# Kernel optimization log

Hardware: AMD Instinct MI355X
Metric: run time of the kernel (lower is better)

## Reference

```python
import jax, jax.numpy as jnp
import numpy as np

BN_EPS = 1e-5
DIM = 256
RED = 4
KH, KW = 3, 3


def setup_inputs() -> dict:
    key = jax.random.key(0)
    ks = jax.random.split(key, 4)
    b, c, h, w = 32, DIM, 64, 64
    hid = DIM // RED
    x = jax.random.normal(ks[0], (b, c, h, w), dtype=jnp.float32)
    # 1x1 convs are just matmuls on pooled [b, c] vectors; store as [out, in]
    w1 = jax.random.normal(ks[1], (hid, c), dtype=jnp.float32) * (1.0 / np.sqrt(c))
    bn_gamma = jnp.ones((hid,), dtype=jnp.float32)
    bn_beta = jnp.zeros((hid,), dtype=jnp.float32)
    bn_mean = jnp.zeros((hid,), dtype=jnp.float32)
    bn_var = jnp.ones((hid,), dtype=jnp.float32)
    w2 = jax.random.normal(ks[2], (c * KH * KW, hid), dtype=jnp.float32) * (1.0 / np.sqrt(hid))
    b2 = jnp.zeros((c * KH * KW,), dtype=jnp.float32)
    bias = jnp.zeros((c,), dtype=jnp.float32)
    return {"x": x, "w1": w1, "bn_gamma": bn_gamma, "bn_beta": bn_beta,
            "bn_mean": bn_mean, "bn_var": bn_var, "w2": w2, "b2": b2, "bias": bias}


def reference(x, w1, bn_gamma, bn_beta, bn_mean, bn_var, w2, b2, bias):
    b, c, h, w = x.shape
    # --- SE-style dynamic weight generation ---
    pooled = jnp.mean(x, axis=(2, 3))                      # [b, c]
    y = jnp.einsum('bc,rc->br', pooled, w1)                # conv1 (1x1, no bias)
    y = (y - bn_mean) * jax.lax.rsqrt(bn_var + BN_EPS) * bn_gamma + bn_beta
    y = jax.nn.sigmoid(y)                                  # note: relu is defined but unused in forward
    dyn = jnp.einsum('br,kr->bk', y, w2) + b2              # [b, c*KH*KW]
    dyn = dyn.reshape(b * c, 1, KH, KW)                    # per-sample depthwise kernels (OIHW)
    # --- per-sample depthwise conv via batch-as-groups trick ---
    out = jax.lax.conv_general_dilated(
        x.reshape(1, b * c, h, w), dyn,
        window_strides=(1, 1), padding=((1, 1), (1, 1)),
        feature_group_count=b * c,
        dimension_numbers=('NCHW', 'OIHW', 'NCHW'))
    out = out.reshape(b, c, h, w) + bias[None, :, None, None]
    return out
```

## Files before the change

### kernel.cpp

```cpp
#include <hip/hip_runtime.h>
#include <hip/hip_bf16.h>

#define DIM 256
#define HID 64
#define HW 4096
#define KK 2304
#define LW 72

typedef float f4 __attribute__((ext_vector_type(4)));

__device__ __forceinline__ int skew_of(int R) {
    int r3 = R & 3;
    int g = (r3 & 2) ? r3 : 0;
    return ((R >> 2) + g) & 3;
}

__global__ __launch_bounds__(256) void pool_kernel(const float* __restrict__ x,
                                                   float* __restrict__ pooled) {
    int plane = blockIdx.x;
    const float4* p = (const float4*)(x + (size_t)plane * HW);
    int tid = threadIdx.x;
    float s = 0.f;
#pragma unroll
    for (int k = 0; k < 4; ++k) {
        float4 v = p[tid + k * 256];
        s += (v.x + v.y) + (v.z + v.w);
    }
#pragma unroll
    for (int off = 32; off > 0; off >>= 1) s += __shfl_down(s, off, 64);
    __shared__ float ws[4];
    int wid = tid >> 6, lane = tid & 63;
    if (lane == 0) ws[wid] = s;
    __syncthreads();
    if (tid == 0) {
        float t = (ws[0] + ws[1]) + (ws[2] + ws[3]);
        pooled[plane] = t * (1.0f / (float)HW);
    }
}

__global__ __launch_bounds__(64) void sig_kernel(const float* __restrict__ pooled,
                                                 const float* __restrict__ w1,
                                                 const float* __restrict__ gamma,
                                                 const float* __restrict__ beta,
                                                 const float* __restrict__ mean,
                                                 const float* __restrict__ var,
                                                 float* __restrict__ sigg) {
    int b = blockIdx.x;
    int t = threadIdx.x;
    __shared__ float sp[DIM];
    ((float4*)sp)[t] = ((const float4*)(pooled + b * DIM))[t];
    __syncthreads();
    const float4* wr = (const float4*)(w1 + t * DIM);
    const float4* s4 = (const float4*)sp;
    float acc = 0.f;
#pragma unroll
    for (int i = 0; i < DIM / 4; ++i) {
        float4 v = wr[i]; float4 u = s4[i];
        acc += v.x * u.x + v.y * u.y + v.z * u.z + v.w * u.w;
    }
    float yb = (acc - mean[t]) * rsqrtf(var[t] + 1e-5f) * gamma[t] + beta[t];
    sigg[b * HID + t] = 1.0f / (1.0f + expf(-yb));
}

__global__ __launch_bounds__(256) void conv_kernel(const float* __restrict__ x,
                                                   const float* __restrict__ sigg,
                                                   const float* __restrict__ w2,
                                                   const float* __restrict__ b2,
                                                   const float* __restrict__ bias,
                                                   float* __restrict__ out) {
    int plane = blockIdx.x;
    int c = plane & (DIM - 1);
    int b = plane >> 8;
    int tid = threadIdx.x;
    const float* xp = x + (size_t)plane * HW;

    __shared__ float lds[66 * LW];
    __shared__ float wsh[12];

    const f4* xp4 = (const f4*)xp;
    f4 st[4];
#pragma unroll
    for (int k = 0; k < 4; ++k) st[k] = __builtin_nontemporal_load(&xp4[tid + k * 256]);

    if (tid < 9) {
        int kk = c * 9 + tid;
        const float4* wk = (const float4*)(w2 + (size_t)kk * HID);
        const float4* sg = (const float4*)(sigg + b * HID);
        float acc = b2[kk];
#pragma unroll
        for (int i = 0; i < HID / 4; ++i) {
            float4 v = wk[i]; float4 u = sg[i];
            acc += v.x * u.x + v.y * u.y + v.z * u.z + v.w * u.w;
        }
        wsh[tid] = acc;
    }

    for (int i = tid; i < 272; i += 256) {
        int addr;
        if (i < 72)        addr = i;
        else if (i < 144)  addr = 65 * LW + (i - 72);
        else {
            int z = i - 144;
            int R = 1 + (z >> 1);
            addr = R * LW + skew_of(R) + 3 + (z & 1) * 65;
        }
        lds[addr] = 0.f;
    }

#pragma unroll
    for (int k = 0; k < 4; ++k) {
        int idx = tid + k * 256;
        int R = (idx >> 4) + 1;
        int col0 = (idx & 15) * 4;
        float* dst = &lds[R * LW + skew_of(R) + 4 + col0];
        dst[0] = st[k].x; dst[1] = st[k].y; dst[2] = st[k].z; dst[3] = st[k].w;
    }
    __syncthreads();

    float w[9];
#pragma unroll
    for (int i = 0; i < 9; ++i) w[i] = wsh[i];
    float bv = bias[c];

    int u = tid >> 4, j = tid & 15;
    float acc[4][4];
#pragma unroll
    for (int m = 0; m < 4; ++m)
#pragma unroll
        for (int i = 0; i < 4; ++i) acc[m][i] = bv;

#define CONTRIB(m, t)                                                          \
    {                                                                          \
        float w0 = w[(t)*3 + 0], w1v = w[(t)*3 + 1], w2v = w[(t)*3 + 2];       \
        acc[m][0] += w0 * a0 + w1v * a1 + w2v * a2;                            \
        acc[m][1] += w0 * a1 + w1v * a2 + w2v * a3;                            \
        acc[m][2] += w0 * a2 + w1v * a3 + w2v * a4;                            \
        acc[m][3] += w0 * a3 + w1v * a4 + w2v * a5;                            \
    }
#define READROW(d)                                                             \
    float a0, a1, a2, a3, a4, a5;                                              \
    {                                                                          \
        int R = 4 * u + (d);                                                   \
        const float* r = &lds[R * LW + skew_of(R) + 3 + 4 * j];                \
        a0 = r[0]; a1 = r[1]; a2 = r[2]; a3 = r[3]; a4 = r[4]; a5 = r[5];      \
    }

    { READROW(0) CONTRIB(0, 0) }
    { READROW(1) CONTRIB(0, 1) CONTRIB(1, 0) }
    { READROW(2) CONTRIB(0, 2) CONTRIB(1, 1) CONTRIB(2, 0) }
    { READROW(3) CONTRIB(1, 2) CONTRIB(2, 1) CONTRIB(3, 0) }
    { READROW(4) CONTRIB(2, 2) CONTRIB(3, 1) }
    { READROW(5) CONTRIB(3, 2) }
#undef READROW
#undef CONTRIB

    f4* op4 = (f4*)(out + (size_t)plane * HW);
#pragma unroll
    for (int m = 0; m < 4; ++m) {
        f4 o;
        o.x = acc[m][0]; o.y = acc[m][1]; o.z = acc[m][2]; o.w = acc[m][3];
        __builtin_nontemporal_store(o, &op4[(4 * u + m) * 16 + j]);
    }
}

extern "C" void kernel_launch(void* const* d_in, const int* in_sizes, int n_in,
                              void* d_out, int out_size, void* d_ws, size_t ws_size,
                              hipStream_t stream) {
    const float* x     = (const float*)d_in[0];
    const float* w1    = (const float*)d_in[1];
    const float* gamma = (const float*)d_in[2];
    const float* beta  = (const float*)d_in[3];
    const float* mean  = (const float*)d_in[4];
    const float* var   = (const float*)d_in[5];
    const float* w2    = (const float*)d_in[6];
    const float* b2    = (const float*)d_in[7];
    const float* bias  = (const float*)d_in[8];
    float* out = (float*)d_out;

    float* pooled = (float*)d_ws;
    float* sigg = pooled + 8192;

    pool_kernel<<<8192, 256, 0, stream>>>(x, pooled);
    sig_kernel<<<32, 64, 0, stream>>>(pooled, w1, gamma, beta, mean, var, sigg);
    conv_kernel<<<8192, 256, 0, stream>>>(x, sigg, w2, b2, bias, out);
}
```

Before: 69.38 us.

## Fuse pool, SE and depthwise conv into one cooperative grid-synced kernel

Replaces the three-kernel pipeline with one cooperative kernel of 1024 blocks, each owning 8 channel planes. Each block loads its planes once, pools them, writes the pooled sums, waits on a grid-wide sync, computes the SE weights and then convolves from data held in registers and LDS. The aim is to avoid reading x twice from HBM and to save two launches. To fit in registers, two of the eight planes are kept as bf16, which loses precision on their conv inputs, and the grid sync plus high register pressure may limit overlap.

```diff
diff --git a/kernel.cpp b/kernel.cpp
--- a/kernel.cpp
+++ b/kernel.cpp
@@ -1,11 +1,11 @@
 #include <hip/hip_runtime.h>
-#include <hip/hip_bf16.h>
+#include <hip/hip_cooperative_groups.h>
 
 #define DIM 256
 #define HID 64
 #define HW 4096
-#define KK 2304
 #define LW 72
+#define PLN 4752
 
 typedef float f4 __attribute__((ext_vector_type(4)));
 
@@ -13,6 +13,203 @@
     int r3 = R & 3;
     int g = (r3 & 2) ? r3 : 0;
     return ((R >> 2) + g) & 3;
+}
+
+__device__ __forceinline__ unsigned int pack_bf16(float a, float b) {
+    unsigned int ua = __float_as_uint(a); ua += 0x7FFFu + ((ua >> 16) & 1u);
+    unsigned int ub = __float_as_uint(b); ub += 0x7FFFu + ((ub >> 16) & 1u);
+    return (ua >> 16) | (ub & 0xFFFF0000u);
+}
+
+__global__ __launch_bounds__(256, 4) void fused_kernel(
+    const float* __restrict__ x, const float* __restrict__ w1,
+    const float* __restrict__ gamma, const float* __restrict__ beta,
+    const float* __restrict__ mean, const float* __restrict__ var,
+    const float* __restrict__ w2, const float* __restrict__ b2,
+    const float* __restrict__ bias, float* __restrict__ out,
+    float* __restrict__ pooled)
+{
+    __shared__ float planes[2][PLN];
+    __shared__ float pp_l[8][4];
+    __shared__ __align__(16) float sp_l[DIM];
+    __shared__ __align__(16) float sig_l[HID];
+    __shared__ float wsh[8][9];
+    __shared__ float bsh[8];
+
+    const int bid = blockIdx.x;
+    const int tid = threadIdx.x;
+    const int b = bid >> 5;
+    const int cbase = (bid & 31) * 8;
+    const size_t plane0 = (size_t)bid * 8;
+    const f4* xb = (const f4*)x + plane0 * (HW / 4);
+
+    for (int i = tid; i < 2 * 272; i += 256) {
+        int q = i / 272, z = i - q * 272;
+        int addr;
+        if (z < 72)        addr = z;
+        else if (z < 144)  addr = 65 * LW + (z - 72);
+        else { int y = z - 144; int R = 1 + (y >> 1);
+               addr = R * LW + skew_of(R) + 3 + (y & 1) * 65; }
+        planes[q][addr] = 0.f;
+    }
+
+#define LDP(pl, k) xb[(size_t)(pl) * 1024 + tid + (k) * 256]
+#define STG1(q, k, v) { int R_ = (tid >> 4) + 16 * (k) + 1;                    \
+    float* d_ = &planes[q][R_ * LW + skew_of(R_) + 4 + (tid & 15) * 4];        \
+    d_[0] = (v).x; d_[1] = (v).y; d_[2] = (v).z; d_[3] = (v).w; }
+#define POOLP(pl, s0, s1, s2, s3) {                                            \
+    float s_ = ((s0.x + s0.y) + (s0.z + s0.w)) + ((s1.x + s1.y) + (s1.z + s1.w)) \
+             + ((s2.x + s2.y) + (s2.z + s2.w)) + ((s3.x + s3.y) + (s3.z + s3.w)); \
+    s_ += __shfl_down(s_, 32, 64); s_ += __shfl_down(s_, 16, 64);              \
+    s_ += __shfl_down(s_, 8, 64);  s_ += __shfl_down(s_, 4, 64);               \
+    s_ += __shfl_down(s_, 2, 64);  s_ += __shfl_down(s_, 1, 64);               \
+    if ((tid & 63) == 0) pp_l[pl][tid >> 6] = s_; }
+
+    f4 rp0[4], rp1[4], rp2[4], rp3[4];
+    unsigned int hp6[8], hp7[8];
+#pragma unroll
+    for (int k = 0; k < 4; ++k) rp0[k] = LDP(0, k);
+    POOLP(0, rp0[0], rp0[1], rp0[2], rp0[3])
+#pragma unroll
+    for (int k = 0; k < 4; ++k) rp1[k] = LDP(1, k);
+    POOLP(1, rp1[0], rp1[1], rp1[2], rp1[3])
+#pragma unroll
+    for (int k = 0; k < 4; ++k) rp2[k] = LDP(2, k);
+    POOLP(2, rp2[0], rp2[1], rp2[2], rp2[3])
+#pragma unroll
+    for (int k = 0; k < 4; ++k) rp3[k] = LDP(3, k);
+    POOLP(3, rp3[0], rp3[1], rp3[2], rp3[3])
+    {
+        f4 t0 = LDP(4, 0), t1 = LDP(4, 1), t2 = LDP(4, 2), t3 = LDP(4, 3);
+        STG1(0, 0, t0) STG1(0, 1, t1) STG1(0, 2, t2) STG1(0, 3, t3)
+        POOLP(4, t0, t1, t2, t3)
+    }
+    {
+        f4 t0 = LDP(5, 0), t1 = LDP(5, 1), t2 = LDP(5, 2), t3 = LDP(5, 3);
+        STG1(1, 0, t0) STG1(1, 1, t1) STG1(1, 2, t2) STG1(1, 3, t3)
+        POOLP(5, t0, t1, t2, t3)
+    }
+    {
+        f4 t0 = LDP(6, 0), t1 = LDP(6, 1), t2 = LDP(6, 2), t3 = LDP(6, 3);
+        POOLP(6, t0, t1, t2, t3)
+        hp6[0] = pack_bf16(t0.x, t0.y); hp6[1] = pack_bf16(t0.z, t0.w);
+        hp6[2] = pack_bf16(t1.x, t1.y); hp6[3] = pack_bf16(t1.z, t1.w);
+        hp6[4] = pack_bf16(t2.x, t2.y); hp6[5] = pack_bf16(t2.z, t2.w);
+        hp6[6] = pack_bf16(t3.x, t3.y); hp6[7] = pack_bf16(t3.z, t3.w);
+    }
+    {
+        f4 t0 = LDP(7, 0), t1 = LDP(7, 1), t2 = LDP(7, 2), t3 = LDP(7, 3);
+        POOLP(7, t0, t1, t2, t3)
+        hp7[0] = pack_bf16(t0.x, t0.y); hp7[1] = pack_bf16(t0.z, t0.w);
+        hp7[2] = pack_bf16(t1.x, t1.y); hp7[3] = pack_bf16(t1.z, t1.w);
+        hp7[4] = pack_bf16(t2.x, t2.y); hp7[5] = pack_bf16(t2.z, t2.w);
+        hp7[6] = pack_bf16(t3.x, t3.y); hp7[7] = pack_bf16(t3.z, t3.w);
+    }
+    __syncthreads();
+    if (tid < 8) {
+        float s = pp_l[tid][0] + pp_l[tid][1] + pp_l[tid][2] + pp_l[tid][3];
+        pooled[plane0 + tid] = s * (1.0f / 4096.0f);
+    }
+
+    cooperative_groups::this_grid().sync();
+
+    sp_l[tid] = pooled[(size_t)b * DIM + tid];
+    __syncthreads();
+    if (tid < 64) {
+        const f4* wr = (const f4*)(w1 + (size_t)tid * DIM);
+        const f4* s4 = (const f4*)sp_l;
+        float acc = 0.f;
+#pragma unroll
+        for (int i = 0; i < DIM / 4; ++i) {
+            f4 v = wr[i], u_ = s4[i];
+            acc += v.x * u_.x + v.y * u_.y + v.z * u_.z + v.w * u_.w;
+        }
+        float yb = (acc - mean[tid]) * rsqrtf(var[tid] + 1e-5f) * gamma[tid] + beta[tid];
+        sig_l[tid] = 1.0f / (1.0f + expf(-yb));
+    }
+    __syncthreads();
+    if (tid < 72) {
+        int pl = tid / 9, tap = tid - pl * 9;
+        int kk = (cbase + pl) * 9 + tap;
+        const f4* wk = (const f4*)(w2 + (size_t)kk * HID);
+        const f4* sg = (const f4*)sig_l;
+        float acc = b2[kk];
+#pragma unroll
+        for (int i = 0; i < HID / 4; ++i) {
+            f4 v = wk[i], u_ = sg[i];
+            acc += v.x * u_.x + v.y * u_.y + v.z * u_.z + v.w * u_.w;
+        }
+        wsh[pl][tap] = acc;
+    } else if (tid < 80) {
+        bsh[tid - 72] = bias[cbase + (tid - 72)];
+    }
+    __syncthreads();
+
+    const int u = tid >> 4, j = tid & 15;
+
+#define RD(d) float a0, a1, a2, a3, a4, a5; { int R_ = 4 * u + (d);            \
+    const float* r_ = &buf_[R_ * LW + skew_of(R_) + 3 + 4 * j];                \
+    a0 = r_[0]; a1 = r_[1]; a2 = r_[2]; a3 = r_[3]; a4 = r_[4]; a5 = r_[5]; }
+#define CT(m, t) { float W0 = wr_[(t)*3], W1 = wr_[(t)*3+1], W2 = wr_[(t)*3+2];\
+    acc_[m][0] += W0*a0 + W1*a1 + W2*a2; acc_[m][1] += W0*a1 + W1*a2 + W2*a3;  \
+    acc_[m][2] += W0*a2 + W1*a3 + W2*a4; acc_[m][3] += W0*a3 + W1*a4 + W2*a5; }
+#define COMPUTE(pl, q) {                                                       \
+    const float* buf_ = planes[q];                                             \
+    float wr_[9];                                                              \
+    _Pragma("unroll") for (int i_ = 0; i_ < 9; ++i_) wr_[i_] = wsh[pl][i_];    \
+    float bv_ = bsh[pl];                                                       \
+    float acc_[4][4];                                                          \
+    _Pragma("unroll") for (int m_ = 0; m_ < 4; ++m_)                           \
+        _Pragma("unroll") for (int i_ = 0; i_ < 4; ++i_) acc_[m_][i_] = bv_;   \
+    { RD(0) CT(0, 0) } { RD(1) CT(0, 1) CT(1, 0) }                             \
+    { RD(2) CT(0, 2) CT(1, 1) CT(2, 0) } { RD(3) CT(1, 2) CT(2, 1) CT(3, 0) }  \
+    { RD(4) CT(2, 2) CT(3, 1) } { RD(5) CT(3, 2) }                             \
+    f4* op4_ = (f4*)(out + (plane0 + (pl)) * (size_t)HW);                      \
+    _Pragma("unroll") for (int m_ = 0; m_ < 4; ++m_) { f4 o_;                  \
+        o_.x = acc_[m_][0]; o_.y = acc_[m_][1];                                \
+        o_.z = acc_[m_][2]; o_.w = acc_[m_][3];                                \
+        __builtin_nontemporal_store(o_, &op4_[(4 * u + m_) * 16 + j]); } }
+
+    COMPUTE(4, 0) COMPUTE(5, 1)
+    __syncthreads();
+#pragma unroll
+    for (int k = 0; k < 4; ++k) { STG1(0, k, rp0[k]) }
+#pragma unroll
+    for (int k = 0; k < 4; ++k) { STG1(1, k, rp1[k]) }
+    __syncthreads();
+    COMPUTE(0, 0) COMPUTE(1, 1)
+    __syncthreads();
+#pragma unroll
+    for (int k = 0; k < 4; ++k) { STG1(0, k, rp2[k]) }
+#pragma unroll
+    for (int k = 0; k < 4; ++k) { STG1(1, k, rp3[k]) }
+    __syncthreads();
+    COMPUTE(2, 0) COMPUTE(3, 1)
+    __syncthreads();
+#pragma unroll
+    for (int k = 0; k < 4; ++k) {
+        f4 t; t.x = __uint_as_float(hp6[2*k] << 16);
+        t.y = __uint_as_float(hp6[2*k] & 0xFFFF0000u);
+        t.z = __uint_as_float(hp6[2*k+1] << 16);
+        t.w = __uint_as_float(hp6[2*k+1] & 0xFFFF0000u);
+        STG1(0, k, t)
+    }
+#pragma unroll
+    for (int k = 0; k < 4; ++k) {
+        f4 t; t.x = __uint_as_float(hp7[2*k] << 16);
+        t.y = __uint_as_float(hp7[2*k] & 0xFFFF0000u);
+        t.z = __uint_as_float(hp7[2*k+1] << 16);
+        t.w = __uint_as_float(hp7[2*k+1] & 0xFFFF0000u);
+        STG1(1, k, t)
+    }
+    __syncthreads();
+    COMPUTE(6, 0) COMPUTE(7, 1)
+#undef LDP
+#undef STG1
+#undef POOLP
+#undef RD
+#undef CT
+#undef COMPUTE
 }
 
 __global__ __launch_bounds__(256) void pool_kernel(const float* __restrict__ x,
@@ -129,7 +326,7 @@
 #pragma unroll
         for (int i = 0; i < 4; ++i) acc[m][i] = bv;
 
-#define CONTRIB(m, t)                                                          \
+#define FCT(m, t)                                                              \
     {                                                                          \
         float w0 = w[(t)*3 + 0], w1v = w[(t)*3 + 1], w2v = w[(t)*3 + 2];       \
         acc[m][0] += w0 * a0 + w1v * a1 + w2v * a2;                            \
@@ -137,7 +334,7 @@
         acc[m][2] += w0 * a2 + w1v * a3 + w2v * a4;                            \
         acc[m][3] += w0 * a3 + w1v * a4 + w2v * a5;                            \
     }
-#define READROW(d)                                                             \
+#define FRD(d)                                                                 \
     float a0, a1, a2, a3, a4, a5;                                              \
     {                                                                          \
         int R = 4 * u + (d);                                                   \
@@ -145,14 +342,14 @@
         a0 = r[0]; a1 = r[1]; a2 = r[2]; a3 = r[3]; a4 = r[4]; a5 = r[5];      \
     }
 
-    { READROW(0) CONTRIB(0, 0) }
-    { READROW(1) CONTRIB(0, 1) CONTRIB(1, 0) }
-    { READROW(2) CONTRIB(0, 2) CONTRIB(1, 1) CONTRIB(2, 0) }
-    { READROW(3) CONTRIB(1, 2) CONTRIB(2, 1) CONTRIB(3, 0) }
-    { READROW(4) CONTRIB(2, 2) CONTRIB(3, 1) }
-    { READROW(5) CONTRIB(3, 2) }
-#undef READROW
-#undef CONTRIB
+    { FRD(0) FCT(0, 0) }
+    { FRD(1) FCT(0, 1) FCT(1, 0) }
+    { FRD(2) FCT(0, 2) FCT(1, 1) FCT(2, 0) }
+    { FRD(3) FCT(1, 2) FCT(2, 1) FCT(3, 0) }
+    { FRD(4) FCT(2, 2) FCT(3, 1) }
+    { FRD(5) FCT(3, 2) }
+#undef FRD
+#undef FCT
 
     f4* op4 = (f4*)(out + (size_t)plane * HW);
 #pragma unroll
@@ -180,6 +377,21 @@
     float* pooled = (float*)d_ws;
     float* sigg = pooled + 8192;
 
+    int nb = 0;
+    hipError_t qe = hipOccupancyMaxActiveBlocksPerMultiprocessor(
+        &nb, (const void*)fused_kernel, 256, 0);
+    if (qe == hipSuccess && nb >= 4) {
+        const float* xa = x; float* oa = out; float* pa = pooled;
+        void* args[11];
+        args[0] = &xa;   args[1] = &w1;  args[2] = &gamma; args[3] = &beta;
+        args[4] = &mean; args[5] = &var; args[6] = &w2;    args[7] = &b2;
+        args[8] = &bias; args[9] = &oa;  args[10] = &pa;
+        hipError_t le = hipLaunchCooperativeKernel((const void*)fused_kernel,
+                                                   dim3(1024), dim3(256),
+                                                   args, 0, stream);
+        if (le == hipSuccess) return;
+    }
+
     pool_kernel<<<8192, 256, 0, stream>>>(x, pooled);
     sig_kernel<<<32, 64, 0, stream>>>(pooled, w1, gamma, beta, mean, var, sigg);
     conv_kernel<<<8192, 256, 0, stream>>>(x, sigg, w2, b2, bias, out);
```

New measurement: 68.62 us. Within noise of the previous version (-1.1%).

## Fuse sigmoid stage into conv kernel, reverse block order for cache reuse

Applied to the files above, without the earlier changes.

Removes the separate sig_kernel launch. Each conv block now recomputes the 64-wide w1·pooled + BN + sigmoid vector into shared memory, at the cost of redundant per-block work (64 threads doing 256-length dot products) and an extra barrier. The conv grid is traversed in reverse plane order so that the planes pool_kernel touched last are read first, and the x loads are switched from nontemporal to normal loads. Together these aim to hit x in the last-level cache after the pooling pass.

```diff
diff --git a/kernel.cpp b/kernel.cpp
--- a/kernel.cpp
+++ b/kernel.cpp
@@ -1,10 +1,8 @@
 #include <hip/hip_runtime.h>
-#include <hip/hip_bf16.h>
 
 #define DIM 256
 #define HID 64
 #define HW 4096
-#define KK 2304
 #define LW 72
 
 typedef float f4 __attribute__((ext_vector_type(4)));
@@ -38,59 +36,55 @@
     }
 }
 
-__global__ __launch_bounds__(64) void sig_kernel(const float* __restrict__ pooled,
-                                                 const float* __restrict__ w1,
-                                                 const float* __restrict__ gamma,
-                                                 const float* __restrict__ beta,
-                                                 const float* __restrict__ mean,
-                                                 const float* __restrict__ var,
-                                                 float* __restrict__ sigg) {
-    int b = blockIdx.x;
-    int t = threadIdx.x;
-    __shared__ float sp[DIM];
-    ((float4*)sp)[t] = ((const float4*)(pooled + b * DIM))[t];
-    __syncthreads();
-    const float4* wr = (const float4*)(w1 + t * DIM);
-    const float4* s4 = (const float4*)sp;
-    float acc = 0.f;
-#pragma unroll
-    for (int i = 0; i < DIM / 4; ++i) {
-        float4 v = wr[i]; float4 u = s4[i];
-        acc += v.x * u.x + v.y * u.y + v.z * u.z + v.w * u.w;
-    }
-    float yb = (acc - mean[t]) * rsqrtf(var[t] + 1e-5f) * gamma[t] + beta[t];
-    sigg[b * HID + t] = 1.0f / (1.0f + expf(-yb));
-}
-
 __global__ __launch_bounds__(256) void conv_kernel(const float* __restrict__ x,
-                                                   const float* __restrict__ sigg,
+                                                   const float* __restrict__ pooled,
+                                                   const float* __restrict__ w1,
+                                                   const float* __restrict__ gamma,
+                                                   const float* __restrict__ beta,
+                                                   const float* __restrict__ mean,
+                                                   const float* __restrict__ var,
                                                    const float* __restrict__ w2,
                                                    const float* __restrict__ b2,
                                                    const float* __restrict__ bias,
                                                    float* __restrict__ out) {
-    int plane = blockIdx.x;
+    int plane = 8191 - (int)blockIdx.x;
     int c = plane & (DIM - 1);
     int b = plane >> 8;
     int tid = threadIdx.x;
     const float* xp = x + (size_t)plane * HW;
 
     __shared__ float lds[66 * LW];
+    __shared__ __align__(16) float sig_l[HID];
     __shared__ float wsh[12];
 
     const f4* xp4 = (const f4*)xp;
     f4 st[4];
 #pragma unroll
-    for (int k = 0; k < 4; ++k) st[k] = __builtin_nontemporal_load(&xp4[tid + k * 256]);
+    for (int k = 0; k < 4; ++k) st[k] = xp4[tid + k * 256];
+
+    if (tid < 64) {
+        const f4* wr = (const f4*)(w1 + (size_t)tid * DIM);
+        const f4* pp = (const f4*)(pooled + (size_t)b * DIM);
+        float acc = 0.f;
+#pragma unroll
+        for (int i = 0; i < DIM / 4; ++i) {
+            f4 v = wr[i], u_ = pp[i];
+            acc += v.x * u_.x + v.y * u_.y + v.z * u_.z + v.w * u_.w;
+        }
+        float yb = (acc - mean[tid]) * rsqrtf(var[tid] + 1e-5f) * gamma[tid] + beta[tid];
+        sig_l[tid] = 1.0f / (1.0f + expf(-yb));
+    }
+    __syncthreads();
 
     if (tid < 9) {
         int kk = c * 9 + tid;
-        const float4* wk = (const float4*)(w2 + (size_t)kk * HID);
-        const float4* sg = (const float4*)(sigg + b * HID);
+        const f4* wk = (const f4*)(w2 + (size_t)kk * HID);
+        const f4* sg = (const f4*)sig_l;
         float acc = b2[kk];
 #pragma unroll
         for (int i = 0; i < HID / 4; ++i) {
-            float4 v = wk[i]; float4 u = sg[i];
-            acc += v.x * u.x + v.y * u.y + v.z * u.z + v.w * u.w;
+            f4 v = wk[i], u_ = sg[i];
+            acc += v.x * u_.x + v.y * u_.y + v.z * u_.z + v.w * u_.w;
         }
         wsh[tid] = acc;
     }
@@ -129,7 +123,7 @@
 #pragma unroll
         for (int i = 0; i < 4; ++i) acc[m][i] = bv;
 
-#define CONTRIB(m, t)                                                          \
+#define FCT(m, t)                                                              \
     {                                                                          \
         float w0 = w[(t)*3 + 0], w1v = w[(t)*3 + 1], w2v = w[(t)*3 + 2];       \
         acc[m][0] += w0 * a0 + w1v * a1 + w2v * a2;                            \
@@ -137,7 +131,7 @@
         acc[m][2] += w0 * a2 + w1v * a3 + w2v * a4;                            \
         acc[m][3] += w0 * a3 + w1v * a4 + w2v * a5;                            \
     }
-#define READROW(d)                                                             \
+#define FRD(d)                                                                 \
     float a0, a1, a2, a3, a4, a5;                                              \
     {                                                                          \
         int R = 4 * u + (d);                                                   \
@@ -145,14 +139,14 @@
         a0 = r[0]; a1 = r[1]; a2 = r[2]; a3 = r[3]; a4 = r[4]; a5 = r[5];      \
     }
 
-    { READROW(0) CONTRIB(0, 0) }
-    { READROW(1) CONTRIB(0, 1) CONTRIB(1, 0) }
-    { READROW(2) CONTRIB(0, 2) CONTRIB(1, 1) CONTRIB(2, 0) }
-    { READROW(3) CONTRIB(1, 2) CONTRIB(2, 1) CONTRIB(3, 0) }
-    { READROW(4) CONTRIB(2, 2) CONTRIB(3, 1) }
-    { READROW(5) CONTRIB(3, 2) }
-#undef READROW
-#undef CONTRIB
+    { FRD(0) FCT(0, 0) }
+    { FRD(1) FCT(0, 1) FCT(1, 0) }
+    { FRD(2) FCT(0, 2) FCT(1, 1) FCT(2, 0) }
+    { FRD(3) FCT(1, 2) FCT(2, 1) FCT(3, 0) }
+    { FRD(4) FCT(2, 2) FCT(3, 1) }
+    { FRD(5) FCT(3, 2) }
+#undef FRD
+#undef FCT
 
     f4* op4 = (f4*)(out + (size_t)plane * HW);
 #pragma unroll
@@ -178,9 +172,8 @@
     float* out = (float*)d_out;
 
     float* pooled = (float*)d_ws;
-    float* sigg = pooled + 8192;
 
     pool_kernel<<<8192, 256, 0, stream>>>(x, pooled);
-    sig_kernel<<<32, 64, 0, stream>>>(pooled, w1, gamma, beta, mean, var, sigg);
-    conv_kernel<<<8192, 256, 0, stream>>>(x, sigg, w2, b2, bias, out);
+    conv_kernel<<<8192, 256, 0, stream>>>(x, pooled, w1, gamma, beta, mean, var,
+                                          w2, b2, bias, out);
 }
```

After: 117.7 us. 1.7x slower.
